# Kernel tuning notes

Hardware: AMD Instinct MI355X
Metric: run time of the kernel (lower is better)

Reference implementation:

```python
import jax, jax.numpy as jnp
import numpy as np

NUM_GRAPHS = 64
EPS = 1e-5


def setup_inputs() -> dict:
    key = jax.random.key(0)
    ks = jax.random.split(key, 10)
    N, E, D, H = 100000, 600000, 128, 128
    inputs = jax.random.normal(ks[0], (N, D), dtype=jnp.float32)
    edge_index = jax.random.randint(ks[1], (2, E), 0, N, dtype=jnp.int64)
    batch = jnp.sort(jax.random.randint(ks[2], (N,), 0, NUM_GRAPHS, dtype=jnp.int64))
    edge_weight = jax.random.uniform(ks[3], (E,), dtype=jnp.float32)
    # learned params: GCNConv linear (glorot) + bias, GraphNorm affine params
    W = jax.random.normal(ks[4], (D, H), dtype=jnp.float32) * (1.0 / np.sqrt(D))
    b = jnp.zeros((H,), dtype=jnp.float32)
    gn_weight = jnp.ones((H,), dtype=jnp.float32)
    gn_bias = jnp.zeros((H,), dtype=jnp.float32)
    gn_alpha = jnp.ones((H,), dtype=jnp.float32)  # GraphNorm mean_scale
    return {"inputs": inputs, "edge_index": edge_index, "batch": batch,
            "edge_weight": edge_weight, "W": W, "b": b,
            "gn_weight": gn_weight, "gn_bias": gn_bias, "gn_alpha": gn_alpha}


def reference(inputs, edge_index, batch, edge_weight, W, b, gn_weight, gn_bias, gn_alpha):
    N = inputs.shape[0]
    # ---- GCNConv with symmetric normalization and added self-loops ----
    loop = jnp.arange(N, dtype=edge_index.dtype)
    row = jnp.concatenate([edge_index[0], loop])  # source nodes
    col = jnp.concatenate([edge_index[1], loop])  # target nodes
    w = jnp.concatenate([edge_weight, jnp.ones((N,), dtype=edge_weight.dtype)])
    deg = jax.ops.segment_sum(w, col, num_segments=N)  # in-degree (weighted)
    dis = jnp.where(deg > 0, jax.lax.rsqrt(deg), 0.0)
    norm = dis[row] * w * dis[col]  # [E+N]
    x = inputs @ W  # [N, H]
    msg = x[row] * norm[:, None]  # gather + scale
    out = jax.ops.segment_sum(msg, col, num_segments=N) + b  # scatter-add
    # ---- GraphNorm: per-graph mean/var with learnable mean scale alpha ----
    cnt = jax.ops.segment_sum(jnp.ones((N,), dtype=out.dtype), batch,
                              num_segments=NUM_GRAPHS)
    cnt = jnp.maximum(cnt, 1.0)[:, None]  # [G,1]
    mean = jax.ops.segment_sum(out, batch, num_segments=NUM_GRAPHS) / cnt
    sub = out - gn_alpha * mean[batch]
    var = jax.ops.segment_sum(sub * sub, batch, num_segments=NUM_GRAPHS) / cnt
    h = sub * jax.lax.rsqrt(var[batch] + EPS) * gn_weight + gn_bias
    # ---- relu (add_residue=False) + global max pool ----
    h = jax.nn.relu(h)
    flat = jax.ops.segment_max(h, batch, num_segments=NUM_GRAPHS)
    return h, flat
```

## Files before the change

kernel.cpp:

```cpp
#include <hip/hip_runtime.h>
#include <math.h>

typedef float f4 __attribute__((ext_vector_type(4)));
typedef float f2 __attribute__((ext_vector_type(2)));

#define NUM_G 64
#define CH 16
#define EPSV 1e-5f

__device__ inline f4 f4_max(f4 a, f4 b) {
  f4 r;
#pragma unroll
  for (int i = 0; i < 4; ++i) r[i] = fmaxf(a[i], b[i]);
  return r;
}

__global__ void k_init(const int* __restrict__ batch, float* __restrict__ deg,
                       int* __restrict__ ecnt, int* __restrict__ gstart, int N) {
  int n = blockIdx.x * blockDim.x + threadIdx.x;
  if (n >= N) return;
  deg[n] = 1.0f;
  ecnt[n] = 0;
  int bn = batch[n];
  int bp = (n == 0) ? -1 : batch[n - 1];
  for (int g = bp + 1; g <= bn; ++g) gstart[g] = n;
  if (n == N - 1) {
    for (int g = bn + 1; g <= NUM_G; ++g) gstart[g] = N;
  }
}

__global__ void k_deg(const int* __restrict__ col, const float* __restrict__ ew,
                      float* __restrict__ deg, int* __restrict__ ecnt, int E) {
  int e = blockIdx.x * blockDim.x + threadIdx.x;
  if (e >= E) return;
  int c = col[e];
  atomicAdd(&deg[c], ew[e]);
  atomicAdd(&ecnt[c], 1);
}

__global__ __launch_bounds__(256) void k_scanA(const int* __restrict__ ecnt,
                                               int* __restrict__ bsum, int N) {
  __shared__ int sb[256];
  int n = blockIdx.x * 256 + threadIdx.x;
  sb[threadIdx.x] = (n < N) ? ecnt[n] : 0;
  __syncthreads();
  for (int o = 128; o >= 1; o >>= 1) {
    if (threadIdx.x < o) sb[threadIdx.x] += sb[threadIdx.x + o];
    __syncthreads();
  }
  if (threadIdx.x == 0) bsum[blockIdx.x] = sb[0];
}

__global__ __launch_bounds__(1024) void k_scanB(int* __restrict__ bsum,
                                                int* __restrict__ off, int NB, int N) {
  __shared__ int sb[1024];
  int t = threadIdx.x;
  int sc = (NB + 1023) >> 10;
  int s = t * sc, e = min(s + sc, NB);
  int local = 0;
  for (int i = s; i < e; ++i) local += bsum[i];
  sb[t] = local;
  __syncthreads();
  for (int o = 1; o < 1024; o <<= 1) {
    int v = sb[t];
    int a = (t >= o) ? sb[t - o] : 0;
    __syncthreads();
    sb[t] = v + a;
    __syncthreads();
  }
  int running = sb[t] - local;
  for (int i = s; i < e; ++i) {
    int v = bsum[i];
    bsum[i] = running;
    running += v;
  }
  if (t == 0) off[N] = sb[1023];
}

__global__ __launch_bounds__(256) void k_scanC(const int* __restrict__ ecnt,
                                               const int* __restrict__ bsum,
                                               const float* __restrict__ deg,
                                               int* __restrict__ off, int* __restrict__ cursor,
                                               float* __restrict__ dis, int N) {
  __shared__ int sb[256];
  int n = blockIdx.x * 256 + threadIdx.x;
  int v = (n < N) ? ecnt[n] : 0;
  sb[threadIdx.x] = v;
  __syncthreads();
  for (int o = 1; o < 256; o <<= 1) {
    int x = sb[threadIdx.x];
    int a = (threadIdx.x >= o) ? sb[threadIdx.x - o] : 0;
    __syncthreads();
    sb[threadIdx.x] = x + a;
    __syncthreads();
  }
  if (n < N) {
    int ex = bsum[blockIdx.x] + sb[threadIdx.x] - v;
    off[n] = ex;
    cursor[n] = ex;
    float d = deg[n];
    dis[n] = (d > 0.f) ? (1.0f / sqrtf(d)) : 0.f;
  }
}

__global__ __launch_bounds__(256) void k_gemm(const float* __restrict__ in,
                                              const float* __restrict__ Wg,
                                              float* __restrict__ x, int N, int ntiles) {
  __shared__ float Wl[128 * 128];
  f4* Wl4 = (f4*)Wl;
  const f4* Wg4 = (const f4*)Wg;
  for (int i = threadIdx.x; i < 4096; i += 256) Wl4[i] = Wg4[i];
  __syncthreads();
  int lane = threadIdx.x & 31;
  int rp = threadIdx.x >> 5;
  int cg = lane * 4;
  for (int tile = blockIdx.x; tile < ntiles; tile += gridDim.x) {
    int r0 = tile * 16 + rp * 2;
    int r1 = r0 + 1;
    bool ok0 = r0 < N, ok1 = r1 < N;
    const f4* a0p = (const f4*)(in + (size_t)(ok0 ? r0 : 0) * 128);
    const f4* a1p = (const f4*)(in + (size_t)(ok1 ? r1 : 0) * 128);
    f4 acc0 = (f4)0.f, acc1 = (f4)0.f;
#pragma unroll 4
    for (int k4 = 0; k4 < 32; ++k4) {
      f4 a0 = a0p[k4];
      f4 a1 = a1p[k4];
      int kb = k4 * 4;
#pragma unroll
      for (int kk = 0; kk < 4; ++kk) {
        f4 wv = Wl4[((kb + kk) * 128 + cg) >> 2];
        acc0 += a0[kk] * wv;
        acc1 += a1[kk] * wv;
      }
    }
    if (ok0) ((f4*)(x + (size_t)r0 * 128))[lane] = acc0;
    if (ok1) ((f4*)(x + (size_t)r1 * 128))[lane] = acc1;
  }
}

__global__ void k_scatter(const int* __restrict__ row, const int* __restrict__ col,
                          const float* __restrict__ ew, const float* __restrict__ dis,
                          int* __restrict__ cursor, int* __restrict__ srow,
                          float* __restrict__ snorm, int E) {
  int e = blockIdx.x * blockDim.x + threadIdx.x;
  if (e >= E) return;
  int r = row[e], c = col[e];
  float nm = dis[r] * ew[e] * dis[c];
  int p = atomicAdd(&cursor[c], 1);
  srow[p] = r;
  snorm[p] = nm;
}

__global__ __launch_bounds__(256) void k_accum(const float* __restrict__ x,
                                               const float* __restrict__ dis,
                                               const int* __restrict__ off,
                                               const int* __restrict__ srow,
                                               const float* __restrict__ snorm,
                                               const float* __restrict__ bias,
                                               float* __restrict__ out, int N) {
  int lane = threadIdx.x & 63;
  int sub = threadIdx.x >> 6;
  int n = blockIdx.x * 4 + sub;
  if (n >= N) return;
  const f2* x2 = (const f2*)x;
  float dn = dis[n];
  f2 acc0 = x2[(size_t)n * 64 + lane] * (dn * dn);
  f2 acc1 = (f2)0.f;
  int s = off[n], e = off[n + 1];
  int i = s;
  for (; i + 2 <= e; i += 2) {
    int r0 = srow[i], r1 = srow[i + 1];
    float nm0 = snorm[i], nm1 = snorm[i + 1];
    f2 v0 = x2[(size_t)r0 * 64 + lane];
    f2 v1 = x2[(size_t)r1 * 64 + lane];
    acc0 += v0 * nm0;
    acc1 += v1 * nm1;
  }
  if (i < e) acc0 += x2[(size_t)srow[i] * 64 + lane] * snorm[i];
  acc0 += acc1 + ((const f2*)bias)[lane];
  ((f2*)out)[(size_t)n * 64 + lane] = acc0;
}

__global__ __launch_bounds__(256) void k_mean_p(const float* __restrict__ out,
                                                const int* __restrict__ gstart,
                                                float* __restrict__ Smean) {
  int g = blockIdx.x / CH, c = blockIdx.x % CH;
  int s = gstart[g], e = gstart[g + 1];
  int len = e - s;
  int csz = (len + CH - 1) / CH;
  int r0 = s + c * csz, r1 = min(r0 + csz, e);
  int lane = threadIdx.x & 31, rg = threadIdx.x >> 5;
  const f4* out4 = (const f4*)out;
  f4 acc = (f4)0.f;
  for (int r = r0 + rg; r < r1; r += 8) acc += out4[(size_t)r * 32 + lane];
  __shared__ f4 red[256];
  red[threadIdx.x] = acc;
  __syncthreads();
  for (int st = 4; st >= 1; st >>= 1) {
    if (rg < st) red[threadIdx.x] += red[threadIdx.x + st * 32];
    __syncthreads();
  }
  if (rg == 0) ((f4*)Smean)[(size_t)(g * CH + c) * 32 + lane] = red[threadIdx.x];
}

__global__ __launch_bounds__(256) void k_var_p(const float* __restrict__ out,
                                               const int* __restrict__ gstart,
                                               const float* __restrict__ Smean,
                                               const float* __restrict__ alpha,
                                               float* __restrict__ Svar) {
  int g = blockIdx.x / CH, c = blockIdx.x % CH;
  int s = gstart[g], e = gstart[g + 1];
  int len = e - s;
  float inv_cnt = 1.0f / (float)((len < 1) ? 1 : len);
  __shared__ f4 meanl[32];
  int lane = threadIdx.x & 31, rg = threadIdx.x >> 5;
  if (threadIdx.x < 32) {
    f4 m = (f4)0.f;
    for (int cc = 0; cc < CH; ++cc) m += ((const f4*)Smean)[(size_t)(g * CH + cc) * 32 + threadIdx.x];
    meanl[threadIdx.x] = m * inv_cnt;
  }
  __syncthreads();
  int csz = (len + CH - 1) / CH;
  int r0 = s + c * csz, r1 = min(r0 + csz, e);
  f4 am = ((const f4*)alpha)[lane] * meanl[lane];
  const f4* out4 = (const f4*)out;
  f4 acc = (f4)0.f;
  for (int r = r0 + rg; r < r1; r += 8) {
    f4 sb = out4[(size_t)r * 32 + lane] - am;
    acc += sb * sb;
  }
  __shared__ f4 red[256];
  red[threadIdx.x] = acc;
  __syncthreads();
  for (int st = 4; st >= 1; st >>= 1) {
    if (rg < st) red[threadIdx.x] += red[threadIdx.x + st * 32];
    __syncthreads();
  }
  if (rg == 0) ((f4*)Svar)[(size_t)(g * CH + c) * 32 + lane] = red[threadIdx.x];
}

__global__ __launch_bounds__(256) void k_final(float* __restrict__ out,
                                               const int* __restrict__ gstart,
                                               const float* __restrict__ Smean,
                                               const float* __restrict__ Svar,
                                               const float* __restrict__ alpha,
                                               const float* __restrict__ gw,
                                               const float* __restrict__ gb,
                                               float* __restrict__ Pmax) {
  int g = blockIdx.x / CH, c = blockIdx.x % CH;
  int s = gstart[g], e = gstart[g + 1];
  int len = e - s;
  float inv_cnt = 1.0f / (float)((len < 1) ? 1 : len);
  __shared__ f4 meanl[32], istdl[32];
  int lane = threadIdx.x & 31, rg = threadIdx.x >> 5;
  if (threadIdx.x < 32) {
    f4 m = (f4)0.f, v = (f4)0.f;
    for (int cc = 0; cc < CH; ++cc) {
      m += ((const f4*)Smean)[(size_t)(g * CH + cc) * 32 + threadIdx.x];
      v += ((const f4*)Svar)[(size_t)(g * CH + cc) * 32 + threadIdx.x];
    }
    m *= inv_cnt;
    v *= inv_cnt;
    f4 is;
#pragma unroll
    for (int i = 0; i < 4; ++i) is[i] = 1.0f / sqrtf(v[i] + EPSV);
    meanl[threadIdx.x] = m;
    istdl[threadIdx.x] = is;
  }
  __syncthreads();
  int csz = (len + CH - 1) / CH;
  int r0 = s + c * csz, r1 = min(r0 + csz, e);
  f4 am = ((const f4*)alpha)[lane] * meanl[lane];
  f4 is = istdl[lane];
  f4 w4 = ((const f4*)gw)[lane];
  f4 b4 = ((const f4*)gb)[lane];
  f4* out4 = (f4*)out;
  f4 mx = (f4)0.f;
  for (int r = r0 + rg; r < r1; r += 8) {
    f4 o = out4[(size_t)r * 32 + lane];
    f4 h = (o - am) * is * w4 + b4;
    h = f4_max(h, (f4)0.f);
    out4[(size_t)r * 32 + lane] = h;
    mx = f4_max(mx, h);
  }
  __shared__ f4 red[256];
  red[threadIdx.x] = mx;
  __syncthreads();
  for (int st = 4; st >= 1; st >>= 1) {
    if (rg < st) red[threadIdx.x] = f4_max(red[threadIdx.x], red[threadIdx.x + st * 32]);
    __syncthreads();
  }
  if (rg == 0) ((f4*)Pmax)[(size_t)(g * CH + c) * 32 + lane] = red[threadIdx.x];
}

__global__ void k_flat(const float* __restrict__ Pmax, float* __restrict__ flat) {
  int g = blockIdx.x;
  int f = threadIdx.x;
  float m = 0.f;
  for (int c = 0; c < CH; ++c) m = fmaxf(m, Pmax[((size_t)g * CH + c) * 128 + f]);
  flat[g * 128 + f] = m;
}

extern "C" void kernel_launch(void* const* d_in, const int* in_sizes, int n_in,
                              void* d_out, int out_size, void* d_ws, size_t ws_size,
                              hipStream_t stream) {
  const float* inputs = (const float*)d_in[0];
  const int* eidx = (const int*)d_in[1];
  const int* batch = (const int*)d_in[2];
  const float* ew = (const float*)d_in[3];
  const float* Wg = (const float*)d_in[4];
  const float* bias = (const float*)d_in[5];
  const float* gw = (const float*)d_in[6];
  const float* gb = (const float*)d_in[7];
  const float* galpha = (const float*)d_in[8];

  int N = in_sizes[0] / 128;
  int E = in_sizes[1] / 2;
  const int* erow = eidx;
  const int* ecol = eidx + E;

  char* w = (char*)d_ws;
  auto alloc = [&](size_t bytes) {
    char* p = w;
    w += (bytes + 255) & ~(size_t)255;
    return p;
  };
  float* x = (float*)alloc((size_t)N * 128 * 4);
  float* deg = (float*)alloc((size_t)N * 4);
  float* dis = (float*)alloc((size_t)N * 4);
  int* ecnt = (int*)alloc((size_t)N * 4);
  int* off = (int*)alloc((size_t)(N + 1) * 4);
  int* cursor = (int*)alloc((size_t)N * 4);
  int* srow = (int*)alloc((size_t)E * 4);
  float* snorm = (float*)alloc((size_t)E * 4);
  int* gstart = (int*)alloc((size_t)(NUM_G + 1) * 4);
  float* Smean = (float*)alloc((size_t)NUM_G * CH * 128 * 4);
  float* Svar = (float*)alloc((size_t)NUM_G * CH * 128 * 4);
  float* Pmax = (float*)alloc((size_t)NUM_G * CH * 128 * 4);
  int NB = (N + 255) / 256;
  int* bsum = (int*)alloc((size_t)NB * 4);

  float* outh = (float*)d_out;
  float* flat = outh + (size_t)N * 128;

  k_init<<<(N + 255) / 256, 256, 0, stream>>>(batch, deg, ecnt, gstart, N);
  k_deg<<<(E + 255) / 256, 256, 0, stream>>>(ecol, ew, deg, ecnt, E);
  k_scanA<<<NB, 256, 0, stream>>>(ecnt, bsum, N);
  k_scanB<<<1, 1024, 0, stream>>>(bsum, off, NB, N);
  k_scanC<<<NB, 256, 0, stream>>>(ecnt, bsum, deg, off, cursor, dis, N);
  int ntiles = (N + 15) / 16;
  k_gemm<<<1024, 256, 0, stream>>>(inputs, Wg, x, N, ntiles);
  k_scatter<<<(E + 255) / 256, 256, 0, stream>>>(erow, ecol, ew, dis, cursor, srow, snorm, E);
  k_accum<<<(N + 3) / 4, 256, 0, stream>>>(x, dis, off, srow, snorm, bias, outh, N);
  k_mean_p<<<NUM_G * CH, 256, 0, stream>>>(outh, gstart, Smean);
  k_var_p<<<NUM_G * CH, 256, 0, stream>>>(outh, gstart, Smean, galpha, Svar);
  k_final<<<NUM_G * CH, 256, 0, stream>>>(outh, gstart, Smean, Svar, galpha, gw, gb, Pmax);
  k_flat<<<NUM_G, 128, 0, stream>>>(Pmax, flat);
}
```

Measured before the change: 376.0 us.

## Fuse GraphNorm mean/var passes, widen GEMM row blocking, unroll gather by four

GraphNorm's separate mean and variance kernels become one pass that collects sum and sum of squares. The final kernel then derives the alpha-shifted variance algebraically, which removes one full read of the 51MB output. The GEMM now gives each thread four rows in 512-thread blocks with one tile per block, so each shared W load is reused across more rows. The edge gather loop is unrolled to four accumulators for more memory-level parallelism. The sum-of-squares variance formula can lose precision through cancellation, and the larger GEMM blocks raise register pressure.

```diff
diff --git a/kernel.cpp b/kernel.cpp
--- a/kernel.cpp
+++ b/kernel.cpp
@@ -103,38 +103,40 @@
   }
 }
 
-__global__ __launch_bounds__(256) void k_gemm(const float* __restrict__ in,
+__global__ __launch_bounds__(512) void k_gemm(const float* __restrict__ in,
                                               const float* __restrict__ Wg,
                                               float* __restrict__ x, int N, int ntiles) {
   __shared__ float Wl[128 * 128];
   f4* Wl4 = (f4*)Wl;
   const f4* Wg4 = (const f4*)Wg;
-  for (int i = threadIdx.x; i < 4096; i += 256) Wl4[i] = Wg4[i];
+  for (int i = threadIdx.x; i < 4096; i += 512) Wl4[i] = Wg4[i];
   __syncthreads();
   int lane = threadIdx.x & 31;
-  int rp = threadIdx.x >> 5;
-  int cg = lane * 4;
+  int rg = threadIdx.x >> 5;
   for (int tile = blockIdx.x; tile < ntiles; tile += gridDim.x) {
-    int r0 = tile * 16 + rp * 2;
-    int r1 = r0 + 1;
-    bool ok0 = r0 < N, ok1 = r1 < N;
-    const f4* a0p = (const f4*)(in + (size_t)(ok0 ? r0 : 0) * 128);
-    const f4* a1p = (const f4*)(in + (size_t)(ok1 ? r1 : 0) * 128);
-    f4 acc0 = (f4)0.f, acc1 = (f4)0.f;
+    int r0 = tile * 64 + rg * 4;
+    bool ok0 = r0 + 0 < N, ok1 = r0 + 1 < N, ok2 = r0 + 2 < N, ok3 = r0 + 3 < N;
+    const f4* a0 = (const f4*)(in + (size_t)(ok0 ? r0 + 0 : 0) * 128);
+    const f4* a1 = (const f4*)(in + (size_t)(ok1 ? r0 + 1 : 0) * 128);
+    const f4* a2 = (const f4*)(in + (size_t)(ok2 ? r0 + 2 : 0) * 128);
+    const f4* a3 = (const f4*)(in + (size_t)(ok3 ? r0 + 3 : 0) * 128);
+    f4 acc0 = (f4)0.f, acc1 = (f4)0.f, acc2 = (f4)0.f, acc3 = (f4)0.f;
 #pragma unroll 4
     for (int k4 = 0; k4 < 32; ++k4) {
-      f4 a0 = a0p[k4];
-      f4 a1 = a1p[k4];
-      int kb = k4 * 4;
+      f4 a0v = a0[k4], a1v = a1[k4], a2v = a2[k4], a3v = a3[k4];
 #pragma unroll
       for (int kk = 0; kk < 4; ++kk) {
-        f4 wv = Wl4[((kb + kk) * 128 + cg) >> 2];
-        acc0 += a0[kk] * wv;
-        acc1 += a1[kk] * wv;
+        f4 wv = Wl4[(k4 * 4 + kk) * 32 + lane];
+        acc0 += a0v[kk] * wv;
+        acc1 += a1v[kk] * wv;
+        acc2 += a2v[kk] * wv;
+        acc3 += a3v[kk] * wv;
       }
     }
-    if (ok0) ((f4*)(x + (size_t)r0 * 128))[lane] = acc0;
-    if (ok1) ((f4*)(x + (size_t)r1 * 128))[lane] = acc1;
+    if (ok0) ((f4*)(x + (size_t)(r0 + 0) * 128))[lane] = acc0;
+    if (ok1) ((f4*)(x + (size_t)(r0 + 1) * 128))[lane] = acc1;
+    if (ok2) ((f4*)(x + (size_t)(r0 + 2) * 128))[lane] = acc2;
+    if (ok3) ((f4*)(x + (size_t)(r0 + 3) * 128))[lane] = acc3;
   }
 }
 
@@ -165,25 +167,26 @@
   const f2* x2 = (const f2*)x;
   float dn = dis[n];
   f2 acc0 = x2[(size_t)n * 64 + lane] * (dn * dn);
-  f2 acc1 = (f2)0.f;
+  f2 acc1 = (f2)0.f, acc2 = (f2)0.f, acc3 = (f2)0.f;
   int s = off[n], e = off[n + 1];
   int i = s;
-  for (; i + 2 <= e; i += 2) {
-    int r0 = srow[i], r1 = srow[i + 1];
-    float nm0 = snorm[i], nm1 = snorm[i + 1];
-    f2 v0 = x2[(size_t)r0 * 64 + lane];
-    f2 v1 = x2[(size_t)r1 * 64 + lane];
-    acc0 += v0 * nm0;
-    acc1 += v1 * nm1;
-  }
-  if (i < e) acc0 += x2[(size_t)srow[i] * 64 + lane] * snorm[i];
-  acc0 += acc1 + ((const f2*)bias)[lane];
+  for (; i + 4 <= e; i += 4) {
+    int r0 = srow[i], r1 = srow[i + 1], r2 = srow[i + 2], r3 = srow[i + 3];
+    float n0 = snorm[i], n1 = snorm[i + 1], n2 = snorm[i + 2], n3 = snorm[i + 3];
+    acc0 += x2[(size_t)r0 * 64 + lane] * n0;
+    acc1 += x2[(size_t)r1 * 64 + lane] * n1;
+    acc2 += x2[(size_t)r2 * 64 + lane] * n2;
+    acc3 += x2[(size_t)r3 * 64 + lane] * n3;
+  }
+  for (; i < e; ++i) acc0 += x2[(size_t)srow[i] * 64 + lane] * snorm[i];
+  acc0 += (acc1 + acc2) + (acc3 + ((const f2*)bias)[lane]);
   ((f2*)out)[(size_t)n * 64 + lane] = acc0;
 }
 
-__global__ __launch_bounds__(256) void k_mean_p(const float* __restrict__ out,
-                                                const int* __restrict__ gstart,
-                                                float* __restrict__ Smean) {
+__global__ __launch_bounds__(256) void k_stats(const float* __restrict__ out,
+                                               const int* __restrict__ gstart,
+                                               float* __restrict__ Ssum,
+                                               float* __restrict__ Ssq) {
   int g = blockIdx.x / CH, c = blockIdx.x % CH;
   int s = gstart[g], e = gstart[g + 1];
   int len = e - s;
@@ -191,58 +194,33 @@
   int r0 = s + c * csz, r1 = min(r0 + csz, e);
   int lane = threadIdx.x & 31, rg = threadIdx.x >> 5;
   const f4* out4 = (const f4*)out;
-  f4 acc = (f4)0.f;
-  for (int r = r0 + rg; r < r1; r += 8) acc += out4[(size_t)r * 32 + lane];
-  __shared__ f4 red[256];
+  f4 acc = (f4)0.f, accq = (f4)0.f;
+  for (int r = r0 + rg; r < r1; r += 8) {
+    f4 v = out4[(size_t)r * 32 + lane];
+    acc += v;
+    accq += v * v;
+  }
+  __shared__ f4 red[256], redq[256];
   red[threadIdx.x] = acc;
+  redq[threadIdx.x] = accq;
   __syncthreads();
   for (int st = 4; st >= 1; st >>= 1) {
-    if (rg < st) red[threadIdx.x] += red[threadIdx.x + st * 32];
-    __syncthreads();
-  }
-  if (rg == 0) ((f4*)Smean)[(size_t)(g * CH + c) * 32 + lane] = red[threadIdx.x];
-}
-
-__global__ __launch_bounds__(256) void k_var_p(const float* __restrict__ out,
-                                               const int* __restrict__ gstart,
-                                               const float* __restrict__ Smean,
-                                               const float* __restrict__ alpha,
-                                               float* __restrict__ Svar) {
-  int g = blockIdx.x / CH, c = blockIdx.x % CH;
-  int s = gstart[g], e = gstart[g + 1];
-  int len = e - s;
-  float inv_cnt = 1.0f / (float)((len < 1) ? 1 : len);
-  __shared__ f4 meanl[32];
-  int lane = threadIdx.x & 31, rg = threadIdx.x >> 5;
-  if (threadIdx.x < 32) {
-    f4 m = (f4)0.f;
-    for (int cc = 0; cc < CH; ++cc) m += ((const f4*)Smean)[(size_t)(g * CH + cc) * 32 + threadIdx.x];
-    meanl[threadIdx.x] = m * inv_cnt;
-  }
-  __syncthreads();
-  int csz = (len + CH - 1) / CH;
-  int r0 = s + c * csz, r1 = min(r0 + csz, e);
-  f4 am = ((const f4*)alpha)[lane] * meanl[lane];
-  const f4* out4 = (const f4*)out;
-  f4 acc = (f4)0.f;
-  for (int r = r0 + rg; r < r1; r += 8) {
-    f4 sb = out4[(size_t)r * 32 + lane] - am;
-    acc += sb * sb;
-  }
-  __shared__ f4 red[256];
-  red[threadIdx.x] = acc;
-  __syncthreads();
-  for (int st = 4; st >= 1; st >>= 1) {
-    if (rg < st) red[threadIdx.x] += red[threadIdx.x + st * 32];
-    __syncthreads();
-  }
-  if (rg == 0) ((f4*)Svar)[(size_t)(g * CH + c) * 32 + lane] = red[threadIdx.x];
+    if (rg < st) {
+      red[threadIdx.x] += red[threadIdx.x + st * 32];
+      redq[threadIdx.x] += redq[threadIdx.x + st * 32];
+    }
+    __syncthreads();
+  }
+  if (rg == 0) {
+    ((f4*)Ssum)[(size_t)(g * CH + c) * 32 + lane] = red[threadIdx.x];
+    ((f4*)Ssq)[(size_t)(g * CH + c) * 32 + lane] = redq[threadIdx.x];
+  }
 }
 
 __global__ __launch_bounds__(256) void k_final(float* __restrict__ out,
                                                const int* __restrict__ gstart,
-                                               const float* __restrict__ Smean,
-                                               const float* __restrict__ Svar,
+                                               const float* __restrict__ Ssum,
+                                               const float* __restrict__ Ssq,
                                                const float* __restrict__ alpha,
                                                const float* __restrict__ gw,
                                                const float* __restrict__ gb,
@@ -251,26 +229,29 @@
   int s = gstart[g], e = gstart[g + 1];
   int len = e - s;
   float inv_cnt = 1.0f / (float)((len < 1) ? 1 : len);
-  __shared__ f4 meanl[32], istdl[32];
+  __shared__ f4 aml[32], istdl[32];
   int lane = threadIdx.x & 31, rg = threadIdx.x >> 5;
   if (threadIdx.x < 32) {
-    f4 m = (f4)0.f, v = (f4)0.f;
+    f4 m = (f4)0.f, q = (f4)0.f;
     for (int cc = 0; cc < CH; ++cc) {
-      m += ((const f4*)Smean)[(size_t)(g * CH + cc) * 32 + threadIdx.x];
-      v += ((const f4*)Svar)[(size_t)(g * CH + cc) * 32 + threadIdx.x];
+      m += ((const f4*)Ssum)[(size_t)(g * CH + cc) * 32 + threadIdx.x];
+      q += ((const f4*)Ssq)[(size_t)(g * CH + cc) * 32 + threadIdx.x];
     }
     m *= inv_cnt;
-    v *= inv_cnt;
+    q *= inv_cnt;
+    f4 al = ((const f4*)alpha)[threadIdx.x];
+    f4 am = al * m;
+    f4 var = q - 2.0f * am * m + am * am;
     f4 is;
 #pragma unroll
-    for (int i = 0; i < 4; ++i) is[i] = 1.0f / sqrtf(v[i] + EPSV);
-    meanl[threadIdx.x] = m;
+    for (int i = 0; i < 4; ++i) is[i] = 1.0f / sqrtf(var[i] + EPSV);
+    aml[threadIdx.x] = am;
     istdl[threadIdx.x] = is;
   }
   __syncthreads();
   int csz = (len + CH - 1) / CH;
   int r0 = s + c * csz, r1 = min(r0 + csz, e);
-  f4 am = ((const f4*)alpha)[lane] * meanl[lane];
+  f4 am = aml[lane];
   f4 is = istdl[lane];
   f4 w4 = ((const f4*)gw)[lane];
   f4 b4 = ((const f4*)gb)[lane];
@@ -334,8 +315,8 @@
   int* srow = (int*)alloc((size_t)E * 4);
   float* snorm = (float*)alloc((size_t)E * 4);
   int* gstart = (int*)alloc((size_t)(NUM_G + 1) * 4);
-  float* Smean = (float*)alloc((size_t)NUM_G * CH * 128 * 4);
-  float* Svar = (float*)alloc((size_t)NUM_G * CH * 128 * 4);
+  float* Ssum = (float*)alloc((size_t)NUM_G * CH * 128 * 4);
+  float* Ssq = (float*)alloc((size_t)NUM_G * CH * 128 * 4);
   float* Pmax = (float*)alloc((size_t)NUM_G * CH * 128 * 4);
   int NB = (N + 255) / 256;
   int* bsum = (int*)alloc((size_t)NB * 4);
@@ -348,12 +329,11 @@
   k_scanA<<<NB, 256, 0, stream>>>(ecnt, bsum, N);
   k_scanB<<<1, 1024, 0, stream>>>(bsum, off, NB, N);
   k_scanC<<<NB, 256, 0, stream>>>(ecnt, bsum, deg, off, cursor, dis, N);
-  int ntiles = (N + 15) / 16;
-  k_gemm<<<1024, 256, 0, stream>>>(inputs, Wg, x, N, ntiles);
+  int ntiles = (N + 63) / 64;
+  k_gemm<<<ntiles, 512, 0, stream>>>(inputs, Wg, x, N, ntiles);
   k_scatter<<<(E + 255) / 256, 256, 0, stream>>>(erow, ecol, ew, dis, cursor, srow, snorm, E);
   k_accum<<<(N + 3) / 4, 256, 0, stream>>>(x, dis, off, srow, snorm, bias, outh, N);
-  k_mean_p<<<NUM_G * CH, 256, 0, stream>>>(outh, gstart, Smean);
-  k_var_p<<<NUM_G * CH, 256, 0, stream>>>(outh, gstart, Smean, galpha, Svar);
-  k_final<<<NUM_G * CH, 256, 0, stream>>>(outh, gstart, Smean, Svar, galpha, gw, gb, Pmax);
+  k_stats<<<NUM_G * CH, 256, 0, stream>>>(outh, gstart, Ssum, Ssq);
+  k_final<<<NUM_G * CH, 256, 0, stream>>>(outh, gstart, Ssum, Ssq, galpha, gw, gb, Pmax);
   k_flat<<<NUM_G, 128, 0, stream>>>(Pmax, flat);
 }
```

Result: faster. 367.0 us (-2.4%).
